# Kernel tuning notes

Measured on AMD Instinct MI355X. Metric: run time of the kernel, lower is better.

## Reference

```python
import jax, jax.numpy as jnp
import numpy as np

N_NODES = 50000


def _gcn_layer(x, src, dst, W, b, inv_deg):
    # gather src features, scatter-add into dst, right-normalize, then dense transform
    agg = jax.ops.segment_sum(x[src], dst, num_segments=N_NODES)  # [N, F]
    h = agg * inv_deg[:, None]
    return h @ W + b


def setup_inputs() -> dict:
    key = jax.random.key(0)
    ks = jax.random.split(key, 6)
    E = 800000
    x = jax.random.normal(ks[0], (N_NODES, 128), dtype=jnp.float32)
    src = jax.random.randint(ks[1], (E,), 0, N_NODES, dtype=jnp.int64)
    dst = jax.random.randint(ks[2], (E,), 0, N_NODES, dtype=jnp.int64)
    W1 = jax.random.normal(ks[3], (128, 128), dtype=jnp.float32) * (1.0 / np.sqrt(128))
    b1 = jnp.zeros((128,), dtype=jnp.float32)
    W2 = jax.random.normal(ks[4], (128, 64), dtype=jnp.float32) * (1.0 / np.sqrt(128))
    b2 = jnp.zeros((64,), dtype=jnp.float32)
    return {"x": x, "src": src, "dst": dst, "W1": W1, "b1": b1, "W2": W2, "b2": b2}


def reference(x, src, dst, W1, b1, W2, b2):
    # in-degree, clamped to 1 (DGL norm='right')
    deg = jax.ops.segment_sum(jnp.ones_like(dst, dtype=x.dtype), dst, num_segments=N_NODES)
    inv_deg = 1.0 / jnp.maximum(deg, 1.0)
    h = _gcn_layer(x, src, dst, W1, b1, inv_deg)
    h = jax.nn.relu(h)  # Dropout in eval mode == identity
    out = _gcn_layer(h, src, dst, W2, b2, inv_deg)
    return out
```

## Files before the change

### kernel.cpp

```cpp
#include <hip/hip_runtime.h>


constexpr int NNODES = 50000;
constexpr int NEDGES = 800000;
constexpr int NBUCKETS = (NNODES + 255) / 256;
constexpr int ABLOCKS = 200;
constexpr int PER = (NEDGES + ABLOCKS - 1) / ABLOCKS;
constexpr int NB_CAST = NNODES * 128 / 8 / 256;
constexpr int NB_PREP = (128 * 128 + 64 * 128 + 255) / 256;

constexpr size_t SZ_ROWSTART = 50048;
constexpr size_t SZ_INVDEG   = 50048;
constexpr size_t SZ_H        = (size_t)ABLOCKS * 256;
constexpr size_t SZ_LOFS     = (size_t)ABLOCKS * 256;
constexpr size_t SZ_CSR      = NEDGES;
constexpr size_t SZ_TMP      = NEDGES;
constexpr size_t SZ_WT1      = 128 * 128 / 2;
constexpr size_t SZ_WT2      = 64 * 128 / 2;
constexpr size_t SZ_XH       = (size_t)NNODES * 128 / 2;
constexpr size_t SZ_AGGH     = (size_t)NNODES * 128 / 2;
constexpr size_t SZ_Y2H      = (size_t)NNODES * 64 / 2;

constexpr size_t OFF_ROWSTART = 0;
constexpr size_t OFF_INVDEG   = OFF_ROWSTART + SZ_ROWSTART;
constexpr size_t OFF_H        = OFF_INVDEG   + SZ_INVDEG;
constexpr size_t OFF_LOFS     = OFF_H        + SZ_H;
constexpr size_t OFF_CSR      = OFF_LOFS     + SZ_LOFS;
constexpr size_t OFF_TMP      = OFF_CSR      + SZ_CSR;
constexpr size_t OFF_WT1      = OFF_TMP      + SZ_TMP;
constexpr size_t OFF_WT2      = OFF_WT1      + SZ_WT1;
constexpr size_t OFF_XH       = OFF_WT2      + SZ_WT2;
constexpr size_t OFF_AGGH     = OFF_XH       + SZ_XH;
constexpr size_t OFF_Y2H      = OFF_AGGH     + SZ_AGGH;
constexpr size_t WS_WORDS     = OFF_Y2H      + SZ_Y2H;
static_assert(WS_WORDS < 11452800, "exceeds r7-proven workspace size");

typedef unsigned short ushortv8 __attribute__((ext_vector_type(8)));
typedef short bf16x8 __attribute__((ext_vector_type(8)));
typedef float f32x4 __attribute__((ext_vector_type(4)));

static __device__ __forceinline__ unsigned short f2bf(float f) {
    unsigned u = __float_as_uint(f);
    u += 0x7fff + ((u >> 16) & 1);
    return (unsigned short)(u >> 16);
}
static __device__ __forceinline__ float bf2f(unsigned short h) {
    return __uint_as_float((unsigned)h << 16);
}

__global__ __launch_bounds__(256) void setup_kernel(
    const int* __restrict__ src, const int* __restrict__ dst,
    unsigned* __restrict__ tmp, int* __restrict__ H, int* __restrict__ LOFS,
    const float* __restrict__ x, ushortv8* __restrict__ xh,
    const float* __restrict__ W1, const float* __restrict__ W2,
    unsigned short* __restrict__ Wt1, unsigned short* __restrict__ Wt2)
{
    const int blk = blockIdx.x;
    const int t = threadIdx.x;
    if (blk < ABLOCKS) {
        __shared__ int cnt[256];
        __shared__ int ofs[256];
        __shared__ int cur[256];
        cnt[t] = 0;
        __syncthreads();
        const int lo = blk * PER;
        const int hi = min(lo + PER, NEDGES);
        for (int i = lo + t; i < hi; i += 256)
            atomicAdd(&cnt[dst[i] >> 8], 1);
        __syncthreads();
        ofs[t] = cnt[t];
        __syncthreads();
        #pragma unroll
        for (int off = 1; off < 256; off <<= 1) {
            const int o = (t >= off) ? ofs[t - off] : 0;
            __syncthreads();
            ofs[t] += o;
            __syncthreads();
        }
        const int excl = ofs[t] - cnt[t];
        cur[t] = excl;
        H[blk * 256 + t] = cnt[t];
        LOFS[blk * 256 + t] = excl;
        __syncthreads();
        for (int i = lo + t; i < hi; i += 256) {
            const int d = dst[i];
            const unsigned pk = ((unsigned)src[i] << 8) | (unsigned)(d & 255);
            const int pos = lo + atomicAdd(&cur[d >> 8], 1);
            tmp[pos] = pk;
        }
    } else if (blk < ABLOCKS + NB_CAST) {
        const int i = (blk - ABLOCKS) * 256 + t;
        const float4* p = reinterpret_cast<const float4*>(x) + (size_t)i * 2;
        const float4 a = p[0], b = p[1];
        ushortv8 v;
        v[0] = f2bf(a.x); v[1] = f2bf(a.y); v[2] = f2bf(a.z); v[3] = f2bf(a.w);
        v[4] = f2bf(b.x); v[5] = f2bf(b.y); v[6] = f2bf(b.z); v[7] = f2bf(b.w);
        xh[i] = v;
    } else {
        const int i = (blk - ABLOCKS - NB_CAST) * 256 + t;
        if (i < 128 * 128) {
            const int n = i >> 7, k = i & 127;
            Wt1[i] = f2bf(W1[k * 128 + n]);
        } else if (i < 128 * 128 + 64 * 128) {
            const int j = i - 128 * 128;
            const int n = j >> 7, k = j & 127;
            Wt2[j] = f2bf(W2[k * 64 + n]);
        }
    }
}

__global__ __launch_bounds__(256) void partB_kernel(
    const unsigned* __restrict__ tmp, const int* __restrict__ H,
    const int* __restrict__ LOFS, int* __restrict__ csr,
    int* __restrict__ rowStart, float* __restrict__ inv_deg, int nNodes)
{
    __shared__ int cs[256];
    __shared__ int s[256];
    __shared__ int epfx[256];
    __shared__ int base[256];
    __shared__ int cnt[256];
    __shared__ int fill[256];
    const int b = blockIdx.x;
    const int t = threadIdx.x;

    int sum = 0;
    for (int w = 0; w < ABLOCKS; ++w) sum += H[w * 256 + t];
    cs[t] = sum;
    s[t] = sum;
    __syncthreads();
    #pragma unroll
    for (int off = 1; off < 256; off <<= 1) {
        const int o = (t >= off) ? s[t - off] : 0;
        __syncthreads();
        s[t] += o;
        __syncthreads();
    }
    const int gbase = s[b] - cs[b];
    const int total = cs[b];
    __syncthreads();

    const int hv = (t < ABLOCKS) ? H[t * 256 + b] : 0;
    s[t] = hv;
    if (t < ABLOCKS) base[t] = t * PER + LOFS[t * 256 + b];
    cnt[t] = 0;
    __syncthreads();
    #pragma unroll
    for (int off = 1; off < 256; off <<= 1) {
        const int o = (t >= off) ? s[t - off] : 0;
        __syncthreads();
        s[t] += o;
        __syncthreads();
    }
    epfx[t] = s[t] - hv;
    __syncthreads();

    for (int j = t; j < total; j += 256) {
        int loW = 0, hiW = ABLOCKS;
        while (hiW - loW > 1) {
            const int mid = (loW + hiW) >> 1;
            if (epfx[mid] <= j) loW = mid; else hiW = mid;
        }
        const unsigned p = tmp[base[loW] + (j - epfx[loW])];
        atomicAdd(&cnt[p & 255u], 1);
    }
    __syncthreads();
    s[t] = cnt[t];
    __syncthreads();
    #pragma unroll
    for (int off = 1; off < 256; off <<= 1) {
        const int o = (t >= off) ? s[t - off] : 0;
        __syncthreads();
        s[t] += o;
        __syncthreads();
    }
    const int excl = gbase + s[t] - cnt[t];
    const int node = b * 256 + t;
    if (node < nNodes) {
        rowStart[node] = excl;
        inv_deg[node] = 1.0f / fmaxf((float)cnt[t], 1.0f);
    }
    if (b == 0 && t == 0) rowStart[nNodes] = NEDGES;
    fill[t] = excl;
    __syncthreads();

    for (int j = t; j < total; j += 256) {
        int loW = 0, hiW = ABLOCKS;
        while (hiW - loW > 1) {
            const int mid = (loW + hiW) >> 1;
            if (epfx[mid] <= j) loW = mid; else hiW = mid;
        }
        const unsigned p = tmp[base[loW] + (j - epfx[loW])];
        const int pos = atomicAdd(&fill[p & 255u], 1);
        csr[pos] = (int)(p >> 8);
    }
}

template<int F, bool EPI, bool OBF16>
__global__ __launch_bounds__(256) void gather_bf16_kernel(
    const ushortv8* __restrict__ feat, const int* __restrict__ csr,
    const int* __restrict__ rowStart, const float* __restrict__ inv_deg,
    const float* __restrict__ bias, void* __restrict__ outv, int nNodes)
{
    constexpr int LPR = F / 8;
    constexpr int EPW = 64 / LPR;
    const int wid = (blockIdx.x * 256 + threadIdx.x) >> 6;
    if (wid >= nNodes) return;
    const int lane = threadIdx.x & 63;
    const int eslot = lane / LPR;
    const int cg = lane % LPR;
    const int rs = rowStart[wid];
    const int re = rowStart[wid + 1];

    float acc0[8] = {}, acc1[8] = {};
    int j = rs + eslot;
    for (; j + EPW < re; j += 2 * EPW) {
        const int s0 = csr[j];
        const int s1 = csr[j + EPW];
        const ushortv8 v0 = feat[(size_t)s0 * LPR + cg];
        const ushortv8 v1 = feat[(size_t)s1 * LPR + cg];
        #pragma unroll
        for (int t = 0; t < 8; ++t) acc0[t] += bf2f(v0[t]);
        #pragma unroll
        for (int t = 0; t < 8; ++t) acc1[t] += bf2f(v1[t]);
    }
    if (j < re) {
        const int s0 = csr[j];
        const ushortv8 v0 = feat[(size_t)s0 * LPR + cg];
        #pragma unroll
        for (int t = 0; t < 8; ++t) acc0[t] += bf2f(v0[t]);
    }
    #pragma unroll
    for (int t = 0; t < 8; ++t) acc0[t] += acc1[t];

    #pragma unroll
    for (int off = LPR; off < 64; off <<= 1) {
        #pragma unroll
        for (int t = 0; t < 8; ++t) acc0[t] += __shfl_down(acc0[t], off, 64);
    }

    if (lane < LPR) {
        if constexpr (EPI) {
            const float s = inv_deg[wid];
            #pragma unroll
            for (int t = 0; t < 8; ++t) acc0[t] = acc0[t] * s + bias[cg * 8 + t];
        }
        if constexpr (OBF16) {
            ushortv8 ov;
            #pragma unroll
            for (int t = 0; t < 8; ++t) ov[t] = f2bf(acc0[t]);
            *reinterpret_cast<ushortv8*>(
                (unsigned short*)outv + (size_t)wid * F + cg * 8) = ov;
        } else {
            float* o = (float*)outv + (size_t)wid * F + cg * 8;
            *reinterpret_cast<float4*>(o) =
                make_float4(acc0[0], acc0[1], acc0[2], acc0[3]);
            *reinterpret_cast<float4*>(o + 4) =
                make_float4(acc0[4], acc0[5], acc0[6], acc0[7]);
        }
    }
}

__global__ __launch_bounds__(256) void mfma_fused_kernel(
    const ushortv8* __restrict__ A,
    const float* __restrict__ inv_deg,
    const ushortv8* __restrict__ Wt1,
    const float* __restrict__ b1,
    const ushortv8* __restrict__ Wt2,
    unsigned short* __restrict__ y2h,
    int nrows)
{
    constexpr int LDK = 136;
    __shared__ alignas(16) unsigned short lwt1[128][LDK];
    __shared__ alignas(16) unsigned short lwt2[64][LDK];
    __shared__ alignas(16) unsigned short la[64][LDK];

    const int row0 = blockIdx.x * 64;
    const int t = threadIdx.x;

    for (int i = t; i < 128 * 16; i += 256) {
        const int r = i >> 4, c = i & 15;
        *reinterpret_cast<ushortv8*>(&lwt1[r][c * 8]) = Wt1[i];
    }
    for (int i = t; i < 64 * 16; i += 256) {
        const int r = i >> 4, c = i & 15;
        *reinterpret_cast<ushortv8*>(&lwt2[r][c * 8]) = Wt2[i];
    }
    for (int i = t; i < 64 * 16; i += 256) {
        const int r = i >> 4, c = i & 15;
        const int row = row0 + r;
        ushortv8 v = {};
        if (row < nrows) {
            v = A[(size_t)row * 16 + c];
            const float s = inv_deg[row];
            #pragma unroll
            for (int jj = 0; jj < 8; ++jj) v[jj] = f2bf(bf2f(v[jj]) * s);
        }
        *reinterpret_cast<ushortv8*>(&la[r][c * 8]) = v;
    }
    __syncthreads();

    const int wave = t >> 6, lane = t & 63;
    const int m = lane & 15, kg = lane >> 4;

    f32x4 acc1[8] = {};
    #pragma unroll
    for (int kk = 0; kk < 4; ++kk) {
        const bf16x8 af =
            *reinterpret_cast<const bf16x8*>(&la[wave * 16 + m][kk * 32 + kg * 8]);
        #pragma unroll
        for (int n = 0; n < 8; ++n) {
            const bf16x8 bf =
                *reinterpret_cast<const bf16x8*>(&lwt1[n * 16 + m][kk * 32 + kg * 8]);
            acc1[n] = __builtin_amdgcn_mfma_f32_16x16x32_bf16(af, bf, acc1[n], 0, 0, 0);
        }
    }
    #pragma unroll
    for (int n = 0; n < 8; ++n) {
        const float bv = b1[n * 16 + m];
        #pragma unroll
        for (int q = 0; q < 4; ++q) {
            const int r = wave * 16 + kg * 4 + q;
            la[r][n * 16 + m] = f2bf(fmaxf(acc1[n][q] + bv, 0.f));
        }
    }
    __syncthreads();

    f32x4 acc2[4] = {};
    #pragma unroll
    for (int kk = 0; kk < 4; ++kk) {
        const bf16x8 af =
            *reinterpret_cast<const bf16x8*>(&la[wave * 16 + m][kk * 32 + kg * 8]);
        #pragma unroll
        for (int n = 0; n < 4; ++n) {
            const bf16x8 bf =
                *reinterpret_cast<const bf16x8*>(&lwt2[n * 16 + m][kk * 32 + kg * 8]);
            acc2[n] = __builtin_amdgcn_mfma_f32_16x16x32_bf16(af, bf, acc2[n], 0, 0, 0);
        }
    }
    __syncthreads();
    #pragma unroll
    for (int n = 0; n < 4; ++n) {
        #pragma unroll
        for (int q = 0; q < 4; ++q) {
            const int r = wave * 16 + kg * 4 + q;
            la[r][n * 16 + m] = f2bf(acc2[n][q]);
        }
    }
    __syncthreads();
    for (int i = t; i < 64 * 8; i += 256) {
        const int r = i >> 3, c = i & 7;
        const int row = row0 + r;
        if (row < nrows)
            *reinterpret_cast<ushortv8*>(&y2h[(size_t)row * 64 + c * 8]) =
                *reinterpret_cast<const ushortv8*>(&la[r][c * 8]);
    }
}

extern "C" void kernel_launch(void* const* d_in, const int* in_sizes, int n_in,
                              void* d_out, int out_size, void* d_ws, size_t ws_size,
                              hipStream_t stream)
{
    const float* x   = (const float*)d_in[0];
    const int*   src = (const int*)d_in[1];
    const int*   dst = (const int*)d_in[2];
    const float* W1  = (const float*)d_in[3];
    const float* b1  = (const float*)d_in[4];
    const float* W2  = (const float*)d_in[5];
    const float* b2  = (const float*)d_in[6];
    float* out = (float*)d_out;

    float* ws  = (float*)d_ws;
    int*   wsi = (int*)d_ws;
    int*            rowStart = wsi + OFF_ROWSTART;
    float*          invdeg   = ws  + OFF_INVDEG;
    int*            H        = wsi + OFF_H;
    int*            LOFS     = wsi + OFF_LOFS;
    int*            csr      = wsi + OFF_CSR;
    unsigned*       tmp      = (unsigned*)(wsi + OFF_TMP);
    unsigned short* Wt1      = (unsigned short*)(wsi + OFF_WT1);
    unsigned short* Wt2      = (unsigned short*)(wsi + OFF_WT2);
    ushortv8*       xh       = (ushortv8*)(wsi + OFF_XH);
    ushortv8*       aggH     = (ushortv8*)(wsi + OFF_AGGH);
    unsigned short* y2h      = (unsigned short*)(wsi + OFF_Y2H);

    setup_kernel<<<ABLOCKS + NB_CAST + NB_PREP, 256, 0, stream>>>(
        src, dst, tmp, H, LOFS, x, xh, W1, W2, Wt1, Wt2);

    partB_kernel<<<NBUCKETS, 256, 0, stream>>>(
        tmp, H, LOFS, csr, rowStart, invdeg, NNODES);

    gather_bf16_kernel<128, false, true><<<(NNODES + 3) / 4, 256, 0, stream>>>(
        xh, csr, rowStart, nullptr, nullptr, aggH, NNODES);

    mfma_fused_kernel<<<(NNODES + 63) / 64, 256, 0, stream>>>(
        aggH, invdeg, (const ushortv8*)Wt1, b1, (const ushortv8*)Wt2,
        y2h, NNODES);

    gather_bf16_kernel<64, true, false><<<(NNODES + 3) / 4, 256, 0, stream>>>(
        (const ushortv8*)y2h, csr, rowStart, invdeg, b2, out, NNODES);
}
```

Baseline: 123.2 us.

## Quantize input features to per-row int8 for the first-layer gather

The input features are now stored as int8 with a per-row absmax scale instead of bf16, and a new int8 gather kernel dequantizes and accumulates neighbour rows into bf16 aggregates. This halves the bytes moved by the random-access neighbour gather of the first layer, which is bandwidth-bound. In exchange it adds a scale lookup per edge and extra quantization error in the features, which could hurt accuracy against the reference tolerance.

```diff
diff --git a/kernel.cpp b/kernel.cpp
--- a/kernel.cpp
+++ b/kernel.cpp
@@ -6,7 +6,7 @@
 constexpr int NBUCKETS = (NNODES + 255) / 256;
 constexpr int ABLOCKS = 200;
 constexpr int PER = (NEDGES + ABLOCKS - 1) / ABLOCKS;
-constexpr int NB_CAST = NNODES * 128 / 8 / 256;
+constexpr int NB_CAST = NNODES / 16;
 constexpr int NB_PREP = (128 * 128 + 64 * 128 + 255) / 256;
 
 constexpr size_t SZ_ROWSTART = 50048;
@@ -17,7 +17,8 @@
 constexpr size_t SZ_TMP      = NEDGES;
 constexpr size_t SZ_WT1      = 128 * 128 / 2;
 constexpr size_t SZ_WT2      = 64 * 128 / 2;
-constexpr size_t SZ_XH       = (size_t)NNODES * 128 / 2;
+constexpr size_t SZ_SCALEX   = 50048;
+constexpr size_t SZ_XQ       = (size_t)NNODES * 128 / 4;
 constexpr size_t SZ_AGGH     = (size_t)NNODES * 128 / 2;
 constexpr size_t SZ_Y2H      = (size_t)NNODES * 64 / 2;
 
@@ -29,8 +30,9 @@
 constexpr size_t OFF_TMP      = OFF_CSR      + SZ_CSR;
 constexpr size_t OFF_WT1      = OFF_TMP      + SZ_TMP;
 constexpr size_t OFF_WT2      = OFF_WT1      + SZ_WT1;
-constexpr size_t OFF_XH       = OFF_WT2      + SZ_WT2;
-constexpr size_t OFF_AGGH     = OFF_XH       + SZ_XH;
+constexpr size_t OFF_SCALEX   = OFF_WT2      + SZ_WT2;
+constexpr size_t OFF_XQ       = OFF_SCALEX   + SZ_SCALEX;
+constexpr size_t OFF_AGGH     = OFF_XQ       + SZ_XQ;
 constexpr size_t OFF_Y2H      = OFF_AGGH     + SZ_AGGH;
 constexpr size_t WS_WORDS     = OFF_Y2H      + SZ_Y2H;
 static_assert(WS_WORDS < 11452800, "exceeds r7-proven workspace size");
@@ -38,6 +40,8 @@
 typedef unsigned short ushortv8 __attribute__((ext_vector_type(8)));
 typedef short bf16x8 __attribute__((ext_vector_type(8)));
 typedef float f32x4 __attribute__((ext_vector_type(4)));
+typedef signed char charv8 __attribute__((ext_vector_type(8)));
+typedef signed char charv16 __attribute__((ext_vector_type(16)));
 
 static __device__ __forceinline__ unsigned short f2bf(float f) {
     unsigned u = __float_as_uint(f);
@@ -51,7 +55,8 @@
 __global__ __launch_bounds__(256) void setup_kernel(
     const int* __restrict__ src, const int* __restrict__ dst,
     unsigned* __restrict__ tmp, int* __restrict__ H, int* __restrict__ LOFS,
-    const float* __restrict__ x, ushortv8* __restrict__ xh,
+    const float* __restrict__ x, signed char* __restrict__ xq,
+    float* __restrict__ scaleX,
     const float* __restrict__ W1, const float* __restrict__ W2,
     unsigned short* __restrict__ Wt1, unsigned short* __restrict__ Wt2)
 {
@@ -89,13 +94,31 @@
             tmp[pos] = pk;
         }
     } else if (blk < ABLOCKS + NB_CAST) {
-        const int i = (blk - ABLOCKS) * 256 + t;
-        const float4* p = reinterpret_cast<const float4*>(x) + (size_t)i * 2;
-        const float4 a = p[0], b = p[1];
-        ushortv8 v;
-        v[0] = f2bf(a.x); v[1] = f2bf(a.y); v[2] = f2bf(a.z); v[3] = f2bf(a.w);
-        v[4] = f2bf(b.x); v[5] = f2bf(b.y); v[6] = f2bf(b.z); v[7] = f2bf(b.w);
-        xh[i] = v;
+        const int lane = t & 63;
+        const int wave = t >> 6;
+        const int row = (blk - ABLOCKS) * 16 + wave * 4 + (lane >> 4);
+        const int ls = lane & 15;
+        const float4* px =
+            reinterpret_cast<const float4*>(x + (size_t)row * 128 + ls * 8);
+        const float4 a = px[0], b = px[1];
+        float m = fmaxf(
+            fmaxf(fmaxf(fabsf(a.x), fabsf(a.y)), fmaxf(fabsf(a.z), fabsf(a.w))),
+            fmaxf(fmaxf(fabsf(b.x), fabsf(b.y)), fmaxf(fabsf(b.z), fabsf(b.w))));
+        #pragma unroll
+        for (int msk = 1; msk < 16; msk <<= 1)
+            m = fmaxf(m, __shfl_xor(m, msk, 16));
+        const float rs = (m > 0.f) ? 127.0f / m : 0.f;
+        charv8 q;
+        q[0] = (signed char)__float2int_rn(a.x * rs);
+        q[1] = (signed char)__float2int_rn(a.y * rs);
+        q[2] = (signed char)__float2int_rn(a.z * rs);
+        q[3] = (signed char)__float2int_rn(a.w * rs);
+        q[4] = (signed char)__float2int_rn(b.x * rs);
+        q[5] = (signed char)__float2int_rn(b.y * rs);
+        q[6] = (signed char)__float2int_rn(b.z * rs);
+        q[7] = (signed char)__float2int_rn(b.w * rs);
+        *reinterpret_cast<charv8*>(xq + (size_t)row * 128 + ls * 8) = q;
+        if (ls == 0) scaleX[row] = (m > 0.f) ? m / 127.0f : 0.f;
     } else {
         const int i = (blk - ABLOCKS - NB_CAST) * 256 + t;
         if (i < 128 * 128) {
@@ -195,11 +218,68 @@
     }
 }
 
-template<int F, bool EPI, bool OBF16>
+__global__ __launch_bounds__(256) void gather_i8_kernel(
+    const charv16* __restrict__ featq, const float* __restrict__ scaleX,
+    const int* __restrict__ csr, const int* __restrict__ rowStart,
+    ushortv8* __restrict__ aggH, int nNodes)
+{
+    constexpr int LPR = 8;
+    constexpr int EPW = 8;
+    const int wid = (blockIdx.x * 256 + threadIdx.x) >> 6;
+    if (wid >= nNodes) return;
+    const int lane = threadIdx.x & 63;
+    const int eslot = lane / LPR;
+    const int cg = lane % LPR;
+    const int rs = rowStart[wid];
+    const int re = rowStart[wid + 1];
+
+    float acc0[16] = {}, acc1[16] = {};
+    int j = rs + eslot;
+    for (; j + EPW < re; j += 2 * EPW) {
+        const int s0 = csr[j];
+        const int s1 = csr[j + EPW];
+        const charv16 q0 = featq[(size_t)s0 * 8 + cg];
+        const charv16 q1 = featq[(size_t)s1 * 8 + cg];
+        const float sc0 = scaleX[s0];
+        const float sc1 = scaleX[s1];
+        #pragma unroll
+        for (int t = 0; t < 16; ++t) acc0[t] += (float)q0[t] * sc0;
+        #pragma unroll
+        for (int t = 0; t < 16; ++t) acc1[t] += (float)q1[t] * sc1;
+    }
+    if (j < re) {
+        const int s0 = csr[j];
+        const charv16 q0 = featq[(size_t)s0 * 8 + cg];
+        const float sc0 = scaleX[s0];
+        #pragma unroll
+        for (int t = 0; t < 16; ++t) acc0[t] += (float)q0[t] * sc0;
+    }
+    #pragma unroll
+    for (int t = 0; t < 16; ++t) acc0[t] += acc1[t];
+
+    #pragma unroll
+    for (int off = LPR; off < 64; off <<= 1) {
+        #pragma unroll
+        for (int t = 0; t < 16; ++t) acc0[t] += __shfl_down(acc0[t], off, 64);
+    }
+
+    if (lane < LPR) {
+        ushortv8 o0, o1;
+        #pragma unroll
+        for (int t = 0; t < 8; ++t) {
+            o0[t] = f2bf(acc0[t]);
+            o1[t] = f2bf(acc0[t + 8]);
+        }
+        aggH[(size_t)wid * 16 + cg * 2] = o0;
+        aggH[(size_t)wid * 16 + cg * 2 + 1] = o1;
+    }
+}
+
+template<int F, bool EPI>
 __global__ __launch_bounds__(256) void gather_bf16_kernel(
     const ushortv8* __restrict__ feat, const int* __restrict__ csr,
     const int* __restrict__ rowStart, const float* __restrict__ inv_deg,
-    const float* __restrict__ bias, void* __restrict__ outv, int nNodes)
+    const float* __restrict__ bias, float* __restrict__ outv, int nNodes)
 {
     constexpr int LPR = F / 8;
     constexpr int EPW = 64 / LPR;
@@ -244,19 +324,11 @@
             #pragma unroll
             for (int t = 0; t < 8; ++t) acc0[t] = acc0[t] * s + bias[cg * 8 + t];
         }
-        if constexpr (OBF16) {
-            ushortv8 ov;
-            #pragma unroll
-            for (int t = 0; t < 8; ++t) ov[t] = f2bf(acc0[t]);
-            *reinterpret_cast<ushortv8*>(
-                (unsigned short*)outv + (size_t)wid * F + cg * 8) = ov;
-        } else {
-            float* o = (float*)outv + (size_t)wid * F + cg * 8;
-            *reinterpret_cast<float4*>(o) =
-                make_float4(acc0[0], acc0[1], acc0[2], acc0[3]);
-            *reinterpret_cast<float4*>(o + 4) =
-                make_float4(acc0[4], acc0[5], acc0[6], acc0[7]);
-        }
+        float* o = outv + (size_t)wid * F + cg * 8;
+        *reinterpret_cast<float4*>(o) =
+            make_float4(acc0[0], acc0[1], acc0[2], acc0[3]);
+        *reinterpret_cast<float4*>(o + 4) =
+            make_float4(acc0[4], acc0[5], acc0[6], acc0[7]);
     }
 }
 
@@ -379,23 +451,24 @@
     unsigned*       tmp      = (unsigned*)(wsi + OFF_TMP);
     unsigned short* Wt1      = (unsigned short*)(wsi + OFF_WT1);
     unsigned short* Wt2      = (unsigned short*)(wsi + OFF_WT2);
-    ushortv8*       xh       = (ushortv8*)(wsi + OFF_XH);
+    float*          scaleX   = ws  + OFF_SCALEX;
+    signed char*    xq       = (signed char*)(wsi + OFF_XQ);
     ushortv8*       aggH     = (ushortv8*)(wsi + OFF_AGGH);
     unsigned short* y2h      = (unsigned short*)(wsi + OFF_Y2H);
 
     setup_kernel<<<ABLOCKS + NB_CAST + NB_PREP, 256, 0, stream>>>(
-        src, dst, tmp, H, LOFS, x, xh, W1, W2, Wt1, Wt2);
+        src, dst, tmp, H, LOFS, x, xq, scaleX, W1, W2, Wt1, Wt2);
 
     partB_kernel<<<NBUCKETS, 256, 0, stream>>>(
         tmp, H, LOFS, csr, rowStart, invdeg, NNODES);
 
-    gather_bf16_kernel<128, false, true><<<(NNODES + 3) / 4, 256, 0, stream>>>(
-        xh, csr, rowStart, nullptr, nullptr, aggH, NNODES);
+    gather_i8_kernel<<<(NNODES + 3) / 4, 256, 0, stream>>>(
+        (const charv16*)xq, scaleX, csr, rowStart, aggH, NNODES);
 
     mfma_fused_kernel<<<(NNODES + 63) / 64, 256, 0, stream>>>(
         aggH, invdeg, (const ushortv8*)Wt1, b1, (const ushortv8*)Wt2,
         y2h, NNODES);
 
-    gather_bf16_kernel<64, true, false><<<(NNODES + 3) / 4, 256, 0, stream>>>(
+    gather_bf16_kernel<64, true><<<(NNODES + 3) / 4, 256, 0, stream>>>(
         (const ushortv8*)y2h, csr, rowStart, invdeg, b2, out, NNODES);
 }
```

New measurement: 124.6 us. Within noise of the previous version (+1.1%).
